# Optimization experiments

Hardware: AMD Instinct MI355X
Metric: run time of the kernel (lower is better)

The kernel has to match this reference:

```python
import jax, jax.numpy as jnp
import numpy as np

N = 20000      # nodes
E = 320000     # edges (before self-loops)
IN = 128       # in_features
H = 8          # heads
C = 120        # out channels per head
SLOPE = 0.2    # LeakyReLU negative slope (PyG default)


def setup_inputs() -> dict:
    key = jax.random.key(0)
    k = jax.random.split(key, 8)
    x = jax.random.normal(k[0], (N, IN), jnp.float32)
    edge_index = jax.random.randint(k[1], (2, E), 0, N)  # [2,E], row0=src, row1=dst
    W = jax.random.normal(k[2], (IN, H * C), jnp.float32) / np.sqrt(IN)
    att_src = jax.random.normal(k[3], (H, C), jnp.float32) * 0.1
    att_dst = jax.random.normal(k[4], (H, C), jnp.float32) * 0.1
    bias = jnp.zeros((H * C,), jnp.float32)
    fc_w = jax.random.normal(k[5], (H * C, 2), jnp.float32) / np.sqrt(H * C)
    fc_b = jnp.zeros((2,), jnp.float32)
    return dict(x=x, edge_index=edge_index, W=W, att_src=att_src,
                att_dst=att_dst, bias=bias, fc_w=fc_w, fc_b=fc_b)


def reference(x, edge_index, W, att_src, att_dst, bias, fc_w, fc_b):
    n = x.shape[0]
    # add self loops (GATConv default add_self_loops=True)
    loops = jnp.arange(n, dtype=edge_index.dtype)
    ei = jnp.concatenate([edge_index, jnp.stack([loops, loops])], axis=1)
    src, dst = ei[0], ei[1]
    # per-head linear projection: [n, H, C]
    xp = (x @ W).reshape(n, H, C)
    # per-node attention logits
    a_s = jnp.einsum('nhc,hc->nh', xp, att_src)  # [n,H]
    a_d = jnp.einsum('nhc,hc->nh', xp, att_dst)  # [n,H]
    # edge-wise logits + LeakyReLU: [Etot,H]
    e = jax.nn.leaky_relu(a_s[src] + a_d[dst], SLOPE)
    # segment softmax over incoming edges of each destination node
    emax = jax.lax.stop_gradient(jax.ops.segment_max(e, dst, num_segments=n))
    ee = jnp.exp(e - emax[dst])
    denom = jax.ops.segment_sum(ee, dst, num_segments=n)
    alpha = ee / denom[dst]                      # [Etot,H]
    # scatter-aggregate weighted messages: [n,H,C]
    out = jax.ops.segment_sum(alpha[:, :, None] * xp[src], dst, num_segments=n)
    out = out.reshape(n, H * C) + bias           # concat heads + bias
    return out @ fc_w + fc_b                     # final Linear -> [n,2]
```

## Files before the change

### kernel.cpp

```cpp
#include <hip/hip_runtime.h>

#define NN    20000
#define EDGES 320000
#define HH    8
#define CC    120
#define HC    960
#define SLOPE 0.2f
#define BUCKET 64
#define NB    128
#define CH    (EDGES / NB)
#define NPAIR (NN / 2)


__global__ __launch_bounds__(256) void prep_kernel(const float* __restrict__ W,
                                                   const float* __restrict__ att_src,
                                                   const float* __restrict__ att_dst,
                                                   const float* __restrict__ bias,
                                                   const float* __restrict__ fc_w,
                                                   const float* __restrict__ fc_b,
                                                   const int* __restrict__ ei,
                                                   float* __restrict__ U,
                                                   float* __restrict__ cbias,
                                                   unsigned* __restrict__ hist) {
  __shared__ unsigned hsh[NPAIR];
  int t = threadIdx.x, b = blockIdx.x;
  int l = t & 63;
  if (b < 256) {
    int p = b * 4 + (t >> 6);
    int k = p >> 3, h = p & 7;
    const float* wrow = W + (size_t)k * HC + h * CC;
    const float* asv  = att_src + h * CC;
    const float* adv  = att_dst + h * CC;
    const float2* fv  = (const float2*)fc_w + h * CC;
    bool tail = (l < CC - 64);
    float w0 = wrow[l],            w1 = tail ? wrow[64 + l] : 0.f;
    float s0 = asv[l],             s1 = tail ? asv[64 + l] : 0.f;
    float d0 = adv[l],             d1 = tail ? adv[64 + l] : 0.f;
    float2 f0 = fv[l];
    float2 f1 = tail ? fv[64 + l] : make_float2(0.f, 0.f);
    float a_s = w0 * s0 + w1 * s1;
    float a_d = w0 * d0 + w1 * d1;
    float z0  = w0 * f0.x + w1 * f1.x;
    float z1  = w0 * f0.y + w1 * f1.y;
#pragma unroll
    for (int m = 1; m < 64; m <<= 1) {
      a_s += __shfl_xor(a_s, m);
      a_d += __shfl_xor(a_d, m);
      z0  += __shfl_xor(z0, m);
      z1  += __shfl_xor(z1, m);
    }
    if (l == 0) {
      float* u = U + k * 32 + 4 * h;
      u[0] = a_s; u[1] = z0; u[2] = z1; u[3] = a_d;
    }
  } else if (b == 256) {
    if (t < 128) {
      int j = t >> 6;
      float acc = 0.f;
      for (int m = l; m < HC; m += 64) acc = fmaf(bias[m], fc_w[m * 2 + j], acc);
#pragma unroll
      for (int m = 1; m < 64; m <<= 1) acc += __shfl_xor(acc, m);
      if (l == 0) cbias[j] = acc + fc_b[j];
    }
  } else {
    int c = b - 257;
    for (int i = t; i < NPAIR; i += 256) hsh[i] = 0u;
    __syncthreads();
    const int* dsts = ei + EDGES + c * CH;
    for (int i = t; i < CH; i += 256) {
      int d = dsts[i];
      atomicAdd(&hsh[d >> 1], (d & 1) ? (1u << 16) : 1u);
    }
    __syncthreads();
    unsigned* hrow = hist + (size_t)c * NPAIR;
    for (int i = t; i < NPAIR; i += 256) hrow[i] = hsh[i];
  }
}

__global__ __launch_bounds__(256) void scan_kernel(const unsigned* __restrict__ hist,
                                                   unsigned* __restrict__ base,
                                                   unsigned* __restrict__ deg) {
  int j = blockIdx.x * 256 + threadIdx.x;
  if (j >= NPAIR) return;
  unsigned sA = 0, sB = 0;
#pragma unroll 8
  for (int c = 0; c < NB; ++c) {
    unsigned v = hist[(size_t)c * NPAIR + j];
    base[(size_t)c * NPAIR + j] = sA | (sB << 16);
    sA += v & 0xFFFFu;
    sB += v >> 16;
  }
  deg[2 * j]     = sA;
  deg[2 * j + 1] = sB;
}

#define XSTR 132
__global__ __launch_bounds__(128) void projplace_kernel(const float* __restrict__ x,
                                                        const float* __restrict__ U,
                                                        const int* __restrict__ ei,
                                                        const unsigned* __restrict__ base,
                                                        unsigned* __restrict__ list,
                                                        float* __restrict__ P) {
  __shared__ unsigned smem[NPAIR];
  int t = threadIdx.x;
  int b = blockIdx.x;

  if (b < 625) {
    float* xs = (float*)smem;
    float* Us = (float*)smem + 32 * XSTR;
    int n0 = b * 32;
    const float4* xg = (const float4*)(x + (size_t)n0 * 128);
    const float4* U4 = (const float4*)U;
    float4 xv[8], uv[8];
#pragma unroll
    for (int j = 0; j < 8; ++j) xv[j] = xg[t + j * 128];
#pragma unroll
    for (int j = 0; j < 8; ++j) uv[j] = U4[t + j * 128];
#pragma unroll
    for (int j = 0; j < 8; ++j) {
      int i = t + j * 128;
      *(float4*)(xs + (i >> 5) * XSTR + (i & 31) * 4) = xv[j];
      ((float4*)Us)[i] = uv[j];
    }
    __syncthreads();

    int rq = t >> 3, cq = t & 7;
    float a00 = 0.f, a01 = 0.f, a02 = 0.f, a03 = 0.f;
    float a10 = 0.f, a11 = 0.f, a12 = 0.f, a13 = 0.f;
    const float* xr0 = xs + rq * XSTR;
    const float* xr1 = xs + (rq + 16) * XSTR;
#pragma unroll 4
    for (int k4 = 0; k4 < 32; ++k4) {
      float4 xa = *(const float4*)(xr0 + k4 * 4);
      float4 xb = *(const float4*)(xr1 + k4 * 4);
      float4 u0 = *(const float4*)(Us + (k4 * 4 + 0) * 32 + 4 * cq);
      float4 u1 = *(const float4*)(Us + (k4 * 4 + 1) * 32 + 4 * cq);
      float4 u2 = *(const float4*)(Us + (k4 * 4 + 2) * 32 + 4 * cq);
      float4 u3 = *(const float4*)(Us + (k4 * 4 + 3) * 32 + 4 * cq);
      a00 = fmaf(xa.x, u0.x, a00); a01 = fmaf(xa.x, u0.y, a01);
      a02 = fmaf(xa.x, u0.z, a02); a03 = fmaf(xa.x, u0.w, a03);
      a10 = fmaf(xb.x, u0.x, a10); a11 = fmaf(xb.x, u0.y, a11);
      a12 = fmaf(xb.x, u0.z, a12); a13 = fmaf(xb.x, u0.w, a13);
      a00 = fmaf(xa.y, u1.x, a00); a01 = fmaf(xa.y, u1.y, a01);
      a02 = fmaf(xa.y, u1.z, a02); a03 = fmaf(xa.y, u1.w, a03);
      a10 = fmaf(xb.y, u1.x, a10); a11 = fmaf(xb.y, u1.y, a11);
      a12 = fmaf(xb.y, u1.z, a12); a13 = fmaf(xb.y, u1.w, a13);
      a00 = fmaf(xa.z, u2.x, a00); a01 = fmaf(xa.z, u2.y, a01);
      a02 = fmaf(xa.z, u2.z, a02); a03 = fmaf(xa.z, u2.w, a03);
      a10 = fmaf(xb.z, u2.x, a10); a11 = fmaf(xb.z, u2.y, a11);
      a12 = fmaf(xb.z, u2.z, a12); a13 = fmaf(xb.z, u2.w, a13);
      a00 = fmaf(xa.w, u3.x, a00); a01 = fmaf(xa.w, u3.y, a01);
      a02 = fmaf(xa.w, u3.z, a02); a03 = fmaf(xa.w, u3.w, a03);
      a10 = fmaf(xb.w, u3.x, a10); a11 = fmaf(xb.w, u3.y, a11);
      a12 = fmaf(xb.w, u3.z, a12); a13 = fmaf(xb.w, u3.w, a13);
    }
    *(float4*)(P + (size_t)(n0 + rq) * 32 + 4 * cq) =
        make_float4(a00, a01, a02, a03);
    *(float4*)(P + (size_t)(n0 + rq + 16) * 32 + 4 * cq) =
        make_float4(a10, a11, a12, a13);
  } else {
    int c = b - 625;
    for (int i = t; i < NPAIR; i += 128)
      smem[i] = base[(size_t)c * NPAIR + i];
    __syncthreads();
    const int* srcs = ei + c * CH;
    const int* dsts = ei + EDGES + c * CH;
    for (int i = t; i < CH; i += 128) {
      int s = srcs[i], d = dsts[i];
      unsigned old = atomicAdd(&smem[d >> 1], (d & 1) ? (1u << 16) : 1u);
      unsigned slot = (d & 1) ? (old >> 16) : (old & 0xFFFFu);
      list[(size_t)d * BUCKET + slot] = (unsigned)s;
    }
  }
}

__global__ __launch_bounds__(256) void gather_kernel(const unsigned* __restrict__ deg_,
                                                     const unsigned* __restrict__ list,
                                                     const float* __restrict__ P,
                                                     const float* __restrict__ cbias,
                                                     float* __restrict__ out) {
  int t = threadIdx.x;
  int wave = t >> 6;
  int lane = t & 63;
  int h = lane & 7;
  int o = lane >> 3;
  int dst = blockIdx.x * 4 + wave;

  const float* pd = P + (size_t)dst * 32;
  float4 pd4 = *(const float4*)(pd + 4 * h);
  float ad = pd4.w;
  unsigned deg = deg_[dst];
  unsigned rv = list[(size_t)dst * BUCKET + lane];

  float accd = 0.f, acc0 = 0.f, acc1 = 0.f;
  if (o == 0) {
    float v = pd4.x + ad;
    v = (v > 0.f) ? v : SLOPE * v;
    float ex = __expf(v);
    accd = ex;
    acc0 = ex * pd4.y;
    acc1 = ex * pd4.z;
  }

  unsigned e0 = o, e1 = o + 8, e2 = o + 16, e3 = o + 24;
  unsigned s0 = __shfl(rv, (int)e0);
  unsigned s1 = __shfl(rv, (int)e1);
  unsigned s2 = __shfl(rv, (int)e2);
  unsigned s3 = __shfl(rv, (int)e3);
  bool m0 = e0 < deg, m1 = e1 < deg, m2 = e2 < deg, m3 = e3 < deg;
  unsigned a0 = m0 ? s0 : (unsigned)dst;
  unsigned a1 = m1 ? s1 : (unsigned)dst;
  unsigned a2 = m2 ? s2 : (unsigned)dst;
  unsigned a3 = m3 ? s3 : (unsigned)dst;
  float4 q0 = *(const float4*)(P + (size_t)a0 * 32 + 4 * h);
  float4 q1 = *(const float4*)(P + (size_t)a1 * 32 + 4 * h);
  float4 q2 = *(const float4*)(P + (size_t)a2 * 32 + 4 * h);
  float4 q3 = *(const float4*)(P + (size_t)a3 * 32 + 4 * h);
  if (m0) {
    float v = q0.x + ad; v = (v > 0.f) ? v : SLOPE * v;
    float ex = __expf(v);
    accd += ex; acc0 = fmaf(ex, q0.y, acc0); acc1 = fmaf(ex, q0.z, acc1);
  }
  if (m1) {
    float v = q1.x + ad; v = (v > 0.f) ? v : SLOPE * v;
    float ex = __expf(v);
    accd += ex; acc0 = fmaf(ex, q1.y, acc0); acc1 = fmaf(ex, q1.z, acc1);
  }
  if (m2) {
    float v = q2.x + ad; v = (v > 0.f) ? v : SLOPE * v;
    float ex = __expf(v);
    accd += ex; acc0 = fmaf(ex, q2.y, acc0); acc1 = fmaf(ex, q2.z, acc1);
  }
  if (m3) {
    float v = q3.x + ad; v = (v > 0.f) ? v : SLOPE * v;
    float ex = __expf(v);
    accd += ex; acc0 = fmaf(ex, q3.y, acc0); acc1 = fmaf(ex, q3.z, acc1);
  }
  if (deg > 32u) {
    unsigned iters = (deg - 32u + 7u) >> 3;
    unsigned e = 32u + (unsigned)o;
    for (unsigned i = 0; i < iters; ++i, e += 8u) {
      unsigned src = __shfl(rv, (int)e);
      if (e < deg) {
        float4 q = *(const float4*)(P + (size_t)src * 32 + 4 * h);
        float v = q.x + ad; v = (v > 0.f) ? v : SLOPE * v;
        float ex = __expf(v);
        accd += ex; acc0 = fmaf(ex, q.y, acc0); acc1 = fmaf(ex, q.z, acc1);
      }
    }
  }
  float accd_tot = accd + __shfl_xor(accd, 8);
  accd_tot += __shfl_xor(accd_tot, 16);
  accd_tot += __shfl_xor(accd_tot, 32);
  float rcp = 1.0f / accd_tot;
  float r0 = acc0 * rcp;
  float r1 = acc1 * rcp;
#pragma unroll
  for (int m = 1; m < 64; m <<= 1) {
    r0 += __shfl_xor(r0, m);
    r1 += __shfl_xor(r1, m);
  }
  if (lane == 0) {
    ((float2*)out)[dst] = make_float2(cbias[0] + r0, cbias[1] + r1);
  }
}

extern "C" void kernel_launch(void* const* d_in, const int* in_sizes, int n_in,
                              void* d_out, int out_size, void* d_ws, size_t ws_size,
                              hipStream_t stream) {
  const float* x       = (const float*)d_in[0];
  const int*   ei      = (const int*)d_in[1];
  const float* W       = (const float*)d_in[2];
  const float* att_src = (const float*)d_in[3];
  const float* att_dst = (const float*)d_in[4];
  const float* bias    = (const float*)d_in[5];
  const float* fc_w    = (const float*)d_in[6];
  const float* fc_b    = (const float*)d_in[7];
  float* out = (float*)d_out;

  float*    U     = (float*)d_ws;
  float*    cbias = U + 4096;
  float*    P     = U + 8192;
  unsigned* deg   = (unsigned*)(P + (size_t)NN * 32);
  unsigned* list  = deg + NN;
  unsigned* hist  = list + (size_t)NN * BUCKET;
  unsigned* base  = hist + (size_t)NB * NPAIR;

  prep_kernel<<<385, 256, 0, stream>>>(W, att_src, att_dst, bias, fc_w, fc_b,
                                       ei, U, cbias, hist);
  scan_kernel<<<40, 256, 0, stream>>>(hist, base, deg);
  projplace_kernel<<<753, 128, 0, stream>>>(x, U, ei, base, list, P);
  gather_kernel<<<NN / 4, 256, 0, stream>>>(deg, list, P, cbias, out);
}
```

Before: 45.37 us.

## Record per-edge ranks in histogram pass and place edges without shared atomics

The histogram pass now stores each edge's local rank (the old value returned by its shared-memory atomic) into a global rank array. The placement blocks no longer reload a 10000-entry base row into shared memory and redo the atomics. Instead, each thread handles two edges independently and computes the slot from base plus rank. The chunk count drops from 128 to 64, which halves the hist/base size and the scan length. The cost is an extra global write and read of the rank array, plus uncoalesced lookups into base.

Measured after the change: 38.78 us, median of 2. 14.5% less time.

```diff
diff --git a/kernel.cpp b/kernel.cpp
--- a/kernel.cpp
+++ b/kernel.cpp
@@ -7,7 +7,7 @@
 #define HC    960
 #define SLOPE 0.2f
 #define BUCKET 64
-#define NB    128
+#define NB    64
 #define CH    (EDGES / NB)
 #define NPAIR (NN / 2)
 
@@ -21,7 +21,8 @@
                                                    const int* __restrict__ ei,
                                                    float* __restrict__ U,
                                                    float* __restrict__ cbias,
-                                                   unsigned* __restrict__ hist) {
+                                                   unsigned* __restrict__ hist,
+                                                   unsigned* __restrict__ rank) {
   __shared__ unsigned hsh[NPAIR];
   int t = threadIdx.x, b = blockIdx.x;
   int l = t & 63;
@@ -67,9 +68,11 @@
     for (int i = t; i < NPAIR; i += 256) hsh[i] = 0u;
     __syncthreads();
     const int* dsts = ei + EDGES + c * CH;
+    unsigned* rnk = rank + c * CH;
     for (int i = t; i < CH; i += 256) {
       int d = dsts[i];
-      atomicAdd(&hsh[d >> 1], (d & 1) ? (1u << 16) : 1u);
+      unsigned old = atomicAdd(&hsh[d >> 1], (d & 1) ? (1u << 16) : 1u);
+      rnk[i] = (d & 1) ? (old >> 16) : (old & 0xFFFFu);
     }
     __syncthreads();
     unsigned* hrow = hist + (size_t)c * NPAIR;
@@ -99,79 +102,79 @@
                                                         const float* __restrict__ U,
                                                         const int* __restrict__ ei,
                                                         const unsigned* __restrict__ base,
+                                                        const unsigned* __restrict__ rank,
                                                         unsigned* __restrict__ list,
                                                         float* __restrict__ P) {
-  __shared__ unsigned smem[NPAIR];
   int t = threadIdx.x;
   int b = blockIdx.x;
 
-  if (b < 625) {
-    float* xs = (float*)smem;
-    float* Us = (float*)smem + 32 * XSTR;
-    int n0 = b * 32;
-    const float4* xg = (const float4*)(x + (size_t)n0 * 128);
-    const float4* U4 = (const float4*)U;
-    float4 xv[8], uv[8];
-#pragma unroll
-    for (int j = 0; j < 8; ++j) xv[j] = xg[t + j * 128];
-#pragma unroll
-    for (int j = 0; j < 8; ++j) uv[j] = U4[t + j * 128];
-#pragma unroll
-    for (int j = 0; j < 8; ++j) {
-      int i = t + j * 128;
-      *(float4*)(xs + (i >> 5) * XSTR + (i & 31) * 4) = xv[j];
-      ((float4*)Us)[i] = uv[j];
-    }
-    __syncthreads();
-
-    int rq = t >> 3, cq = t & 7;
-    float a00 = 0.f, a01 = 0.f, a02 = 0.f, a03 = 0.f;
-    float a10 = 0.f, a11 = 0.f, a12 = 0.f, a13 = 0.f;
-    const float* xr0 = xs + rq * XSTR;
-    const float* xr1 = xs + (rq + 16) * XSTR;
+  if (b >= 625) {
+    int e0 = (b - 625) * 256 + t;
+#pragma unroll
+    for (int j = 0; j < 2; ++j) {
+      int e = e0 + j * 128;
+      int d = ei[EDGES + e];
+      unsigned r = rank[e];
+      unsigned c = (unsigned)e / (unsigned)CH;
+      unsigned packed = base[(size_t)c * NPAIR + (d >> 1)];
+      unsigned bs = (d & 1) ? (packed >> 16) : (packed & 0xFFFFu);
+      list[(size_t)d * BUCKET + bs + r] = (unsigned)ei[e];
+    }
+    return;
+  }
+
+  __shared__ float xs[32 * XSTR];
+  __shared__ float Us[128 * 32];
+  int n0 = b * 32;
+  const float4* xg = (const float4*)(x + (size_t)n0 * 128);
+  const float4* U4 = (const float4*)U;
+  float4 xv[8], uv[8];
+#pragma unroll
+  for (int j = 0; j < 8; ++j) xv[j] = xg[t + j * 128];
+#pragma unroll
+  for (int j = 0; j < 8; ++j) uv[j] = U4[t + j * 128];
+#pragma unroll
+  for (int j = 0; j < 8; ++j) {
+    int i = t + j * 128;
+    *(float4*)(xs + (i >> 5) * XSTR + (i & 31) * 4) = xv[j];
+    ((float4*)Us)[i] = uv[j];
+  }
+  __syncthreads();
+
+  int rq = t >> 3, cq = t & 7;
+  float a00 = 0.f, a01 = 0.f, a02 = 0.f, a03 = 0.f;
+  float a10 = 0.f, a11 = 0.f, a12 = 0.f, a13 = 0.f;
+  const float* xr0 = xs + rq * XSTR;
+  const float* xr1 = xs + (rq + 16) * XSTR;
 #pragma unroll 4
-    for (int k4 = 0; k4 < 32; ++k4) {
-      float4 xa = *(const float4*)(xr0 + k4 * 4);
-      float4 xb = *(const float4*)(xr1 + k4 * 4);
-      float4 u0 = *(const float4*)(Us + (k4 * 4 + 0) * 32 + 4 * cq);
-      float4 u1 = *(const float4*)(Us + (k4 * 4 + 1) * 32 + 4 * cq);
-      float4 u2 = *(const float4*)(Us + (k4 * 4 + 2) * 32 + 4 * cq);
-      float4 u3 = *(const float4*)(Us + (k4 * 4 + 3) * 32 + 4 * cq);
-      a00 = fmaf(xa.x, u0.x, a00); a01 = fmaf(xa.x, u0.y, a01);
-      a02 = fmaf(xa.x, u0.z, a02); a03 = fmaf(xa.x, u0.w, a03);
-      a10 = fmaf(xb.x, u0.x, a10); a11 = fmaf(xb.x, u0.y, a11);
-      a12 = fmaf(xb.x, u0.z, a12); a13 = fmaf(xb.x, u0.w, a13);
-      a00 = fmaf(xa.y, u1.x, a00); a01 = fmaf(xa.y, u1.y, a01);
-      a02 = fmaf(xa.y, u1.z, a02); a03 = fmaf(xa.y, u1.w, a03);
-      a10 = fmaf(xb.y, u1.x, a10); a11 = fmaf(xb.y, u1.y, a11);
-      a12 = fmaf(xb.y, u1.z, a12); a13 = fmaf(xb.y, u1.w, a13);
-      a00 = fmaf(xa.z, u2.x, a00); a01 = fmaf(xa.z, u2.y, a01);
-      a02 = fmaf(xa.z, u2.z, a02); a03 = fmaf(xa.z, u2.w, a03);
-      a10 = fmaf(xb.z, u2.x, a10); a11 = fmaf(xb.z, u2.y, a11);
-      a12 = fmaf(xb.z, u2.z, a12); a13 = fmaf(xb.z, u2.w, a13);
-      a00 = fmaf(xa.w, u3.x, a00); a01 = fmaf(xa.w, u3.y, a01);
-      a02 = fmaf(xa.w, u3.z, a02); a03 = fmaf(xa.w, u3.w, a03);
-      a10 = fmaf(xb.w, u3.x, a10); a11 = fmaf(xb.w, u3.y, a11);
-      a12 = fmaf(xb.w, u3.z, a12); a13 = fmaf(xb.w, u3.w, a13);
-    }
-    *(float4*)(P + (size_t)(n0 + rq) * 32 + 4 * cq) =
-        make_float4(a00, a01, a02, a03);
-    *(float4*)(P + (size_t)(n0 + rq + 16) * 32 + 4 * cq) =
-        make_float4(a10, a11, a12, a13);
-  } else {
-    int c = b - 625;
-    for (int i = t; i < NPAIR; i += 128)
-      smem[i] = base[(size_t)c * NPAIR + i];
-    __syncthreads();
-    const int* srcs = ei + c * CH;
-    const int* dsts = ei + EDGES + c * CH;
-    for (int i = t; i < CH; i += 128) {
-      int s = srcs[i], d = dsts[i];
-      unsigned old = atomicAdd(&smem[d >> 1], (d & 1) ? (1u << 16) : 1u);
-      unsigned slot = (d & 1) ? (old >> 16) : (old & 0xFFFFu);
-      list[(size_t)d * BUCKET + slot] = (unsigned)s;
-    }
-  }
+  for (int k4 = 0; k4 < 32; ++k4) {
+    float4 xa = *(const float4*)(xr0 + k4 * 4);
+    float4 xb = *(const float4*)(xr1 + k4 * 4);
+    float4 u0 = *(const float4*)(Us + (k4 * 4 + 0) * 32 + 4 * cq);
+    float4 u1 = *(const float4*)(Us + (k4 * 4 + 1) * 32 + 4 * cq);
+    float4 u2 = *(const float4*)(Us + (k4 * 4 + 2) * 32 + 4 * cq);
+    float4 u3 = *(const float4*)(Us + (k4 * 4 + 3) * 32 + 4 * cq);
+    a00 = fmaf(xa.x, u0.x, a00); a01 = fmaf(xa.x, u0.y, a01);
+    a02 = fmaf(xa.x, u0.z, a02); a03 = fmaf(xa.x, u0.w, a03);
+    a10 = fmaf(xb.x, u0.x, a10); a11 = fmaf(xb.x, u0.y, a11);
+    a12 = fmaf(xb.x, u0.z, a12); a13 = fmaf(xb.x, u0.w, a13);
+    a00 = fmaf(xa.y, u1.x, a00); a01 = fmaf(xa.y, u1.y, a01);
+    a02 = fmaf(xa.y, u1.z, a02); a03 = fmaf(xa.y, u1.w, a03);
+    a10 = fmaf(xb.y, u1.x, a10); a11 = fmaf(xb.y, u1.y, a11);
+    a12 = fmaf(xb.y, u1.z, a12); a13 = fmaf(xb.y, u1.w, a13);
+    a00 = fmaf(xa.z, u2.x, a00); a01 = fmaf(xa.z, u2.y, a01);
+    a02 = fmaf(xa.z, u2.z, a02); a03 = fmaf(xa.z, u2.w, a03);
+    a10 = fmaf(xb.z, u2.x, a10); a11 = fmaf(xb.z, u2.y, a11);
+    a12 = fmaf(xb.z, u2.z, a12); a13 = fmaf(xb.z, u2.w, a13);
+    a00 = fmaf(xa.w, u3.x, a00); a01 = fmaf(xa.w, u3.y, a01);
+    a02 = fmaf(xa.w, u3.z, a02); a03 = fmaf(xa.w, u3.w, a03);
+    a10 = fmaf(xb.w, u3.x, a10); a11 = fmaf(xb.w, u3.y, a11);
+    a12 = fmaf(xb.w, u3.z, a12); a13 = fmaf(xb.w, u3.w, a13);
+  }
+  *(float4*)(P + (size_t)(n0 + rq) * 32 + 4 * cq) =
+      make_float4(a00, a01, a02, a03);
+  *(float4*)(P + (size_t)(n0 + rq + 16) * 32 + 4 * cq) =
+      make_float4(a10, a11, a12, a13);
 }
 
 __global__ __launch_bounds__(256) void gather_kernel(const unsigned* __restrict__ deg_,
@@ -285,10 +288,11 @@
   unsigned* list  = deg + NN;
   unsigned* hist  = list + (size_t)NN * BUCKET;
   unsigned* base  = hist + (size_t)NB * NPAIR;
-
-  prep_kernel<<<385, 256, 0, stream>>>(W, att_src, att_dst, bias, fc_w, fc_b,
-                                       ei, U, cbias, hist);
+  unsigned* rank  = base + (size_t)NB * NPAIR;
+
+  prep_kernel<<<321, 256, 0, stream>>>(W, att_src, att_dst, bias, fc_w, fc_b,
+                                       ei, U, cbias, hist, rank);
   scan_kernel<<<40, 256, 0, stream>>>(hist, base, deg);
-  projplace_kernel<<<753, 128, 0, stream>>>(x, U, ei, base, list, P);
+  projplace_kernel<<<1875, 128, 0, stream>>>(x, U, ei, base, rank, list, P);
   gather_kernel<<<NN / 4, 256, 0, stream>>>(deg, list, P, cbias, out);
 }
```
